# Optimization experiments

Hardware: AMD Instinct MI355X
Metric: run time of the kernel (lower is better)

## Reference

```python
import jax, jax.numpy as jnp
import numpy as np

B, T, E = 2048, 200, 128
H1, H2 = 64, 32
NEG_INF = -(2.0 ** 32) + 1.0  # matches tf source's -2**32 + 1 padding value


def setup_inputs() -> dict:
    key = jax.random.key(0)
    ks = jax.random.split(key, 8)
    queries = jax.random.normal(ks[0], (B, E), dtype=jnp.float32)
    keys = jax.random.normal(ks[1], (B, T, E), dtype=jnp.float32)
    keys_id = jax.random.randint(ks[2], (B, T), 0, 2, dtype=jnp.int32)
    # Dense params: MLP input is concat([q,k,q-k,q*k]) -> 4*E = 512
    W1 = jax.random.normal(ks[3], (4 * E, H1), dtype=jnp.float32) * (1.0 / np.sqrt(4 * E))
    b1 = jnp.zeros((H1,), dtype=jnp.float32)
    W2 = jax.random.normal(ks[4], (H1, H2), dtype=jnp.float32) * (1.0 / np.sqrt(H1))
    b2 = jnp.zeros((H2,), dtype=jnp.float32)
    W3 = jax.random.normal(ks[5], (H2, 1), dtype=jnp.float32) * (1.0 / np.sqrt(H2))
    b3 = jnp.zeros((1,), dtype=jnp.float32)
    return {"queries": queries, "keys": keys, "keys_id": keys_id,
            "W1": W1, "b1": b1, "W2": W2, "b2": b2, "W3": W3, "b3": b3}


def reference(queries, keys, keys_id, W1, b1, W2, b2, W3, b3):
    # tile query over the time axis: [B,E] -> [B,T,E]
    q = jnp.broadcast_to(queries[:, None, :], keys.shape)
    # concat features: [B,T,4E]
    feat = jnp.concatenate([q, keys, q - keys, q * keys], axis=2)
    # small MLP scorer
    h = jax.nn.relu(jnp.einsum('btf,fh->bth', feat, W1) + b1)
    h = jax.nn.relu(jnp.einsum('bth,hk->btk', h, W2) + b2)
    weight = jnp.einsum('btk,ko->bto', h, W3) + b3  # [B,T,1]
    # masked softmax over time axis (padding id == 0)
    mask = (keys_id != 0)[:, :, None]  # [B,T,1]
    weight = jnp.where(mask, weight, jnp.float32(NEG_INF))
    weight = jax.nn.softmax(weight, axis=1)
    # weighted mean pooling (original uses reduce_mean, i.e. sum/T)
    return jnp.mean(weight * keys, axis=1)  # [B,E]
```

## Files before the change

kernel.cpp:

```cpp
#include <hip/hip_runtime.h>

#define NEG_INF_F (-4294967295.0f)

typedef __attribute__((ext_vector_type(8))) short bf16x8;
typedef __attribute__((ext_vector_type(4))) float f32x4;

__device__ __forceinline__ unsigned short f2bf(float x) {
    unsigned u = __float_as_uint(x);
    unsigned r = (u + 0x7fffu + ((u >> 16) & 1u)) >> 16;
    return (unsigned short)r;
}
__device__ __forceinline__ float bf2f(unsigned short s) {
    return __uint_as_float(((unsigned)s) << 16);
}

struct __align__(16) Smem {
    unsigned short K[200 * 128];
    unsigned short h1s[4][16 * 64];
    float q[128];
    float maskf[208];
    float cpart[256];
    float s[208];
    float ppart[128];
    float red[16];
};
static_assert(sizeof(Smem) <= 64 * 1024, "LDS over 64 KiB");

__global__ __launch_bounds__(256, 2)
void attn_fused(const float* __restrict__ Q,
                const float* __restrict__ Kg,
                const int*   __restrict__ kid,
                const float* __restrict__ W1,
                const float* __restrict__ b1,
                const float* __restrict__ W2,
                const float* __restrict__ b2,
                const float* __restrict__ W3,
                const float* __restrict__ b3,
                float* __restrict__ out)
{
    __shared__ Smem sm;
    const int b    = blockIdx.x;
    const int tid  = threadIdx.x;
    const int wave = tid >> 6;
    const int lane = tid & 63;
    const int l15  = lane & 15;
    const int quad = lane >> 4;

    if (tid < 128) sm.q[tid] = Q[b * 128 + tid];
    if (tid < 200) sm.maskf[tid] = (kid[b * 200 + tid] != 0) ? 1.0f : 0.0f;
    __syncthreads();

    {
        const int n = tid & 63, kc = tid >> 6;
        float acc = (kc == 0) ? b1[n] : 0.0f;
        #pragma unroll 4
        for (int i = 0; i < 32; ++i) {
            const int k = kc * 32 + i;
            acc += sm.q[k] * (W1[k * 64 + n] + W1[(256 + k) * 64 + n]);
        }
        sm.cpart[kc * 64 + n] = acc;
    }

    {
        const float4* src = reinterpret_cast<const float4*>(Kg + (size_t)b * 200 * 128);
        #pragma unroll
        for (int r = 0; r < 25; ++r) {
            const int idx4 = tid + 256 * r;
            const float4 v = src[idx4];
            const int t = idx4 >> 5;
            const int e = (idx4 & 31) << 2;
            const int g = (e >> 3) ^ (t & 15);
            ushort4 pk;
            pk.x = f2bf(v.x); pk.y = f2bf(v.y); pk.z = f2bf(v.z); pk.w = f2bf(v.w);
            *reinterpret_cast<ushort4*>(&sm.K[t * 128 + g * 8 + (e & 7)]) = pk;
        }
    }
    __syncthreads();

    bf16x8 Mf[4][4];
    #pragma unroll
    for (int ks = 0; ks < 4; ++ks) {
        #pragma unroll
        for (int nt = 0; nt < 4; ++nt) {
            const int n = nt * 16 + l15;
            const int kb = ks * 32 + quad * 8;
            bf16x8 f;
            #pragma unroll
            for (int j = 0; j < 8; ++j) {
                const int k = kb + j;
                const float wb = W1[(128 + k) * 64 + n];
                const float wd = W1[(256 + k) * 64 + n];
                const float wp = W1[(384 + k) * 64 + n];
                f[j] = (short)f2bf((wb - wd) + sm.q[k] * wp);
            }
            Mf[ks][nt] = f;
        }
    }
    bf16x8 W2f[2][2];
    #pragma unroll
    for (int ks = 0; ks < 2; ++ks) {
        #pragma unroll
        for (int nt = 0; nt < 2; ++nt) {
            const int n = nt * 16 + l15;
            const int kb = ks * 32 + quad * 8;
            bf16x8 f;
            #pragma unroll
            for (int j = 0; j < 8; ++j) f[j] = (short)f2bf(W2[(kb + j) * 32 + n]);
            W2f[ks][nt] = f;
        }
    }
    const float w3a = W3[l15],  w3b = W3[16 + l15];
    const float b2a = b2[l15],  b2b = b2[16 + l15];
    const float b3v = b3[0];
    float cn[4];
    #pragma unroll
    for (int nt = 0; nt < 4; ++nt) {
        const int n = nt * 16 + l15;
        cn[nt] = sm.cpart[n] + sm.cpart[64 + n] + sm.cpart[128 + n] + sm.cpart[192 + n];
    }

    unsigned short* h1w = &sm.h1s[wave][0];
    const f32x4 zero4 = {0.f, 0.f, 0.f, 0.f};

    for (int tile = wave; tile < 13; tile += 4) {
        const int t0 = tile * 16;
        const int t  = t0 + l15;
        f32x4 acc[4] = {zero4, zero4, zero4, zero4};
        #pragma unroll
        for (int ks = 0; ks < 4; ++ks) {
            const int g = (ks * 4 + quad) ^ (t & 15);
            const bf16x8 A = *reinterpret_cast<const bf16x8*>(&sm.K[t * 128 + g * 8]);
            #pragma unroll
            for (int nt = 0; nt < 4; ++nt)
                acc[nt] = __builtin_amdgcn_mfma_f32_16x16x32_bf16(A, Mf[ks][nt], acc[nt], 0, 0, 0);
        }
        #pragma unroll
        for (int nt = 0; nt < 4; ++nt) {
            const int n = nt * 16 + l15;
            #pragma unroll
            for (int r = 0; r < 4; ++r) {
                const int m = quad * 4 + r;
                const float h = fmaxf(acc[nt][r] + cn[nt], 0.0f);
                const int g = (n >> 3) ^ (m & 7);
                h1w[m * 64 + g * 8 + (n & 7)] = f2bf(h);
            }
        }
        f32x4 p0 = zero4, p1 = zero4;
        #pragma unroll
        for (int ks = 0; ks < 2; ++ks) {
            const int g = (ks * 4 + quad) ^ (l15 & 7);
            const bf16x8 A2 = *reinterpret_cast<const bf16x8*>(&h1w[l15 * 64 + g * 8]);
            p0 = __builtin_amdgcn_mfma_f32_16x16x32_bf16(A2, W2f[ks][0], p0, 0, 0, 0);
            p1 = __builtin_amdgcn_mfma_f32_16x16x32_bf16(A2, W2f[ks][1], p1, 0, 0, 0);
        }
        float sv[4];
        #pragma unroll
        for (int r = 0; r < 4; ++r)
            sv[r] = fmaxf(p0[r] + b2a, 0.f) * w3a + fmaxf(p1[r] + b2b, 0.f) * w3b;
        #pragma unroll
        for (int off = 1; off < 16; off <<= 1) {
            #pragma unroll
            for (int r = 0; r < 4; ++r) sv[r] += __shfl_xor(sv[r], off);
        }
        if (l15 == 0) {
            #pragma unroll
            for (int r = 0; r < 4; ++r) {
                const int tt = t0 + quad * 4 + r;
                if (tt < 200)
                    sm.s[tt] = (sm.maskf[tt] != 0.0f) ? (sv[r] + b3v) : NEG_INF_F;
                else if (tt < 208)
                    sm.s[tt] = -__builtin_inff();
            }
        }
    }
    __syncthreads();

    {
        const float v = (tid < 208) ? sm.s[tid] : -__builtin_inff();
        float m = v;
        #pragma unroll
        for (int off = 32; off >= 1; off >>= 1) m = fmaxf(m, __shfl_xor(m, off));
        if (lane == 0) sm.red[wave] = m;
        __syncthreads();
        m = fmaxf(fmaxf(sm.red[0], sm.red[1]), fmaxf(sm.red[2], sm.red[3]));
        const float ev = (tid < 208) ? __expf(v - m) : 0.0f;
        float ssum = ev;
        #pragma unroll
        for (int off = 32; off >= 1; off >>= 1) ssum += __shfl_xor(ssum, off);
        if (lane == 0) sm.red[8 + wave] = ssum;
        __syncthreads();
        const float S = sm.red[8] + sm.red[9] + sm.red[10] + sm.red[11];
        const float inv = 1.0f / (S * 200.0f);
        if (tid < 208) sm.s[tid] = ev * inv;
    }
    __syncthreads();

    {
        const int e = tid & 127;
        const int h = tid >> 7;
        float acc2 = 0.0f;
        const int tbeg = h * 100;
        for (int tt = tbeg; tt < tbeg + 100; ++tt) {
            const float wv = sm.s[tt];
            const int g = (e >> 3) ^ (tt & 15);
            acc2 += wv * bf2f(sm.K[tt * 128 + g * 8 + (e & 7)]);
        }
        if (h == 1) sm.ppart[e] = acc2;
        __syncthreads();
        if (h == 0) out[(size_t)b * 128 + e] = acc2 + sm.ppart[e];
    }
}

extern "C" void kernel_launch(void* const* d_in, const int* in_sizes, int n_in,
                              void* d_out, int out_size, void* d_ws, size_t ws_size,
                              hipStream_t stream) {
    (void)in_sizes; (void)n_in; (void)out_size; (void)d_ws; (void)ws_size;
    attn_fused<<<dim3(2048), dim3(256), 0, stream>>>(
        (const float*)d_in[0], (const float*)d_in[1], (const int*)d_in[2],
        (const float*)d_in[3], (const float*)d_in[4], (const float*)d_in[5],
        (const float*)d_in[6], (const float*)d_in[7], (const float*)d_in[8],
        (float*)d_out);
}
```

Before: 354.0 us.

## Assign one batch row per wave and stream keys from global memory

Each 256-thread block now handles four batch rows, one per wave, and launches 512 blocks instead of 2048. Keys are no longer staged as bf16 in LDS; each wave reads its rows directly from global memory for both the MLP and the pooling pass. The q-dependent weight fold is replaced by a second MFMA per step on q*k against shared Wd/Wp fragments, so the weights are built once per block and shared by the four rows. Softmax runs entirely within a wave with no block barriers. The trade-off is twice the MFMA work, keys read twice from global memory or cache, and fewer blocks available to hide latency.

```diff
diff --git a/kernel.cpp b/kernel.cpp
--- a/kernel.cpp
+++ b/kernel.cpp
@@ -1,4 +1,5 @@
 #include <hip/hip_runtime.h>
+#include <hip/hip_bf16.h>
 
 #define NEG_INF_F (-4294967295.0f)
 
@@ -7,24 +8,22 @@
 
 __device__ __forceinline__ unsigned short f2bf(float x) {
     unsigned u = __float_as_uint(x);
-    unsigned r = (u + 0x7fffu + ((u >> 16) & 1u)) >> 16;
-    return (unsigned short)r;
-}
-__device__ __forceinline__ float bf2f(unsigned short s) {
-    return __uint_as_float(((unsigned)s) << 16);
-}
+    return (unsigned short)((u + 0x7fffu + ((u >> 16) & 1u)) >> 16);
+}
+__device__ __forceinline__ unsigned f2bf2(float a, float b) {
+    __hip_bfloat162 h2 = __float22bfloat162_rn(make_float2(a, b));
+    unsigned r; __builtin_memcpy(&r, &h2, 4); return r;
+}
+
+union FragU { unsigned u[4]; bf16x8 h; };
 
 struct __align__(16) Smem {
-    unsigned short K[200 * 128];
+    unsigned short Wt[2][64 * 128];
     unsigned short h1s[4][16 * 64];
-    float q[128];
-    float maskf[208];
-    float cpart[256];
-    float s[208];
-    float ppart[128];
-    float red[16];
+    float q[4][128];
+    float c[4][64];
+    float w[4][208];
 };
-static_assert(sizeof(Smem) <= 64 * 1024, "LDS over 64 KiB");
 
 __global__ __launch_bounds__(256, 2)
 void attn_fused(const float* __restrict__ Q,
@@ -39,61 +38,49 @@
                 float* __restrict__ out)
 {
     __shared__ Smem sm;
-    const int b    = blockIdx.x;
     const int tid  = threadIdx.x;
     const int wave = tid >> 6;
     const int lane = tid & 63;
     const int l15  = lane & 15;
     const int quad = lane >> 4;
-
-    if (tid < 128) sm.q[tid] = Q[b * 128 + tid];
-    if (tid < 200) sm.maskf[tid] = (kid[b * 200 + tid] != 0) ? 1.0f : 0.0f;
+    const int b    = blockIdx.x * 4 + wave;
+
+    {
+        const int n  = tid & 63;
+        const int ko = tid >> 6;
+        #pragma unroll 8
+        for (int i = 0; i < 32; ++i) {
+            const int k = i * 4 + ko;
+            const float a = W1[(128 + k) * 64 + n];
+            const float d = W1[(256 + k) * 64 + n];
+            const float p = W1[(384 + k) * 64 + n];
+            const int g = (k >> 3) ^ (n & 15);
+            sm.Wt[0][n * 128 + g * 8 + (k & 7)] = f2bf(a - d);
+            sm.Wt[1][n * 128 + g * 8 + (k & 7)] = f2bf(p);
+        }
+    }
+    sm.q[wave][lane]      = Q[b * 128 + lane];
+    sm.q[wave][64 + lane] = Q[b * 128 + 64 + lane];
     __syncthreads();
 
     {
-        const int n = tid & 63, kc = tid >> 6;
-        float acc = (kc == 0) ? b1[n] : 0.0f;
+        const int n = lane;
+        float acc = b1[n];
         #pragma unroll 4
-        for (int i = 0; i < 32; ++i) {
-            const int k = kc * 32 + i;
-            acc += sm.q[k] * (W1[k * 64 + n] + W1[(256 + k) * 64 + n]);
-        }
-        sm.cpart[kc * 64 + n] = acc;
-    }
-
-    {
-        const float4* src = reinterpret_cast<const float4*>(Kg + (size_t)b * 200 * 128);
-        #pragma unroll
-        for (int r = 0; r < 25; ++r) {
-            const int idx4 = tid + 256 * r;
-            const float4 v = src[idx4];
-            const int t = idx4 >> 5;
-            const int e = (idx4 & 31) << 2;
-            const int g = (e >> 3) ^ (t & 15);
-            ushort4 pk;
-            pk.x = f2bf(v.x); pk.y = f2bf(v.y); pk.z = f2bf(v.z); pk.w = f2bf(v.w);
-            *reinterpret_cast<ushort4*>(&sm.K[t * 128 + g * 8 + (e & 7)]) = pk;
-        }
-    }
-    __syncthreads();
-
-    bf16x8 Mf[4][4];
+        for (int k = 0; k < 128; ++k)
+            acc += sm.q[wave][k] * (W1[k * 64 + n] + W1[(256 + k) * 64 + n]);
+        sm.c[wave][n] = acc;
+    }
+
+    bf16x8 Wcf[4][4], Wpf[4][4];
     #pragma unroll
     for (int ks = 0; ks < 4; ++ks) {
         #pragma unroll
         for (int nt = 0; nt < 4; ++nt) {
             const int n = nt * 16 + l15;
-            const int kb = ks * 32 + quad * 8;
-            bf16x8 f;
-            #pragma unroll
-            for (int j = 0; j < 8; ++j) {
-                const int k = kb + j;
-                const float wb = W1[(128 + k) * 64 + n];
-                const float wd = W1[(256 + k) * 64 + n];
-                const float wp = W1[(384 + k) * 64 + n];
-                f[j] = (short)f2bf((wb - wd) + sm.q[k] * wp);
-            }
-            Mf[ks][nt] = f;
+            const int g = (ks * 4 + quad) ^ l15;
+            Wcf[ks][nt] = *reinterpret_cast<const bf16x8*>(&sm.Wt[0][n * 128 + g * 8]);
+            Wpf[ks][nt] = *reinterpret_cast<const bf16x8*>(&sm.Wt[1][n * 128 + g * 8]);
         }
     }
     bf16x8 W2f[2][2];
@@ -112,27 +99,42 @@
     const float w3a = W3[l15],  w3b = W3[16 + l15];
     const float b2a = b2[l15],  b2b = b2[16 + l15];
     const float b3v = b3[0];
+    float4 qa[4], qb[4];
+    #pragma unroll
+    for (int ks = 0; ks < 4; ++ks) {
+        const int e0 = ks * 32 + quad * 8;
+        qa[ks] = *reinterpret_cast<const float4*>(&sm.q[wave][e0]);
+        qb[ks] = *reinterpret_cast<const float4*>(&sm.q[wave][e0 + 4]);
+    }
     float cn[4];
     #pragma unroll
-    for (int nt = 0; nt < 4; ++nt) {
-        const int n = nt * 16 + l15;
-        cn[nt] = sm.cpart[n] + sm.cpart[64 + n] + sm.cpart[128 + n] + sm.cpart[192 + n];
-    }
+    for (int nt = 0; nt < 4; ++nt) cn[nt] = sm.c[wave][nt * 16 + l15];
 
     unsigned short* h1w = &sm.h1s[wave][0];
     const f32x4 zero4 = {0.f, 0.f, 0.f, 0.f};
-
-    for (int tile = wave; tile < 13; tile += 4) {
+    const float* kbase = Kg + (size_t)b * 25600;
+
+    for (int tile = 0; tile < 13; ++tile) {
         const int t0 = tile * 16;
-        const int t  = t0 + l15;
+        const int tr = min(t0 + l15, 199);
+        const float* kr = kbase + tr * 128;
         f32x4 acc[4] = {zero4, zero4, zero4, zero4};
         #pragma unroll
         for (int ks = 0; ks < 4; ++ks) {
-            const int g = (ks * 4 + quad) ^ (t & 15);
-            const bf16x8 A = *reinterpret_cast<const bf16x8*>(&sm.K[t * 128 + g * 8]);
-            #pragma unroll
-            for (int nt = 0; nt < 4; ++nt)
-                acc[nt] = __builtin_amdgcn_mfma_f32_16x16x32_bf16(A, Mf[ks][nt], acc[nt], 0, 0, 0);
+            const float4 k0 = *reinterpret_cast<const float4*>(kr + ks * 32 + quad * 8);
+            const float4 k1 = *reinterpret_cast<const float4*>(kr + ks * 32 + quad * 8 + 4);
+            FragU A1, A2;
+            A1.u[0] = f2bf2(k0.x, k0.y);           A1.u[1] = f2bf2(k0.z, k0.w);
+            A1.u[2] = f2bf2(k1.x, k1.y);           A1.u[3] = f2bf2(k1.z, k1.w);
+            A2.u[0] = f2bf2(k0.x * qa[ks].x, k0.y * qa[ks].y);
+            A2.u[1] = f2bf2(k0.z * qa[ks].z, k0.w * qa[ks].w);
+            A2.u[2] = f2bf2(k1.x * qb[ks].x, k1.y * qb[ks].y);
+            A2.u[3] = f2bf2(k1.z * qb[ks].z, k1.w * qb[ks].w);
+            #pragma unroll
+            for (int nt = 0; nt < 4; ++nt) {
+                acc[nt] = __builtin_amdgcn_mfma_f32_16x16x32_bf16(A1.h, Wcf[ks][nt], acc[nt], 0, 0, 0);
+                acc[nt] = __builtin_amdgcn_mfma_f32_16x16x32_bf16(A2.h, Wpf[ks][nt], acc[nt], 0, 0, 0);
+            }
         }
         #pragma unroll
         for (int nt = 0; nt < 4; ++nt) {
@@ -149,9 +151,9 @@
         #pragma unroll
         for (int ks = 0; ks < 2; ++ks) {
             const int g = (ks * 4 + quad) ^ (l15 & 7);
-            const bf16x8 A2 = *reinterpret_cast<const bf16x8*>(&h1w[l15 * 64 + g * 8]);
-            p0 = __builtin_amdgcn_mfma_f32_16x16x32_bf16(A2, W2f[ks][0], p0, 0, 0, 0);
-            p1 = __builtin_amdgcn_mfma_f32_16x16x32_bf16(A2, W2f[ks][1], p1, 0, 0, 0);
+            const bf16x8 A2l = *reinterpret_cast<const bf16x8*>(&h1w[l15 * 64 + g * 8]);
+            p0 = __builtin_amdgcn_mfma_f32_16x16x32_bf16(A2l, W2f[ks][0], p0, 0, 0, 0);
+            p1 = __builtin_amdgcn_mfma_f32_16x16x32_bf16(A2l, W2f[ks][1], p1, 0, 0, 0);
         }
         float sv[4];
         #pragma unroll
@@ -164,50 +166,60 @@
         }
         if (l15 == 0) {
             #pragma unroll
-            for (int r = 0; r < 4; ++r) {
-                const int tt = t0 + quad * 4 + r;
-                if (tt < 200)
-                    sm.s[tt] = (sm.maskf[tt] != 0.0f) ? (sv[r] + b3v) : NEG_INF_F;
-                else if (tt < 208)
-                    sm.s[tt] = -__builtin_inff();
+            for (int r = 0; r < 4; ++r) sm.w[wave][t0 + quad * 4 + r] = sv[r];
+        }
+    }
+
+    {
+        const float NINF = -__builtin_inff();
+        float v[4];
+        #pragma unroll
+        for (int i = 0; i < 4; ++i) {
+            const int t = lane + i * 64;
+            float x = NINF;
+            if (t < 200) {
+                const float raw = sm.w[wave][t];
+                x = (kid[b * 200 + t] != 0) ? (raw + b3v) : NEG_INF_F;
             }
-        }
-    }
-    __syncthreads();
-
-    {
-        const float v = (tid < 208) ? sm.s[tid] : -__builtin_inff();
-        float m = v;
-        #pragma unroll
-        for (int off = 32; off >= 1; off >>= 1) m = fmaxf(m, __shfl_xor(m, off));
-        if (lane == 0) sm.red[wave] = m;
-        __syncthreads();
-        m = fmaxf(fmaxf(sm.red[0], sm.red[1]), fmaxf(sm.red[2], sm.red[3]));
-        const float ev = (tid < 208) ? __expf(v - m) : 0.0f;
-        float ssum = ev;
-        #pragma unroll
-        for (int off = 32; off >= 1; off >>= 1) ssum += __shfl_xor(ssum, off);
-        if (lane == 0) sm.red[8 + wave] = ssum;
-        __syncthreads();
-        const float S = sm.red[8] + sm.red[9] + sm.red[10] + sm.red[11];
+            v[i] = x;
+        }
+        float m = fmaxf(fmaxf(v[0], v[1]), fmaxf(v[2], v[3]));
+        #pragma unroll
+        for (int off = 1; off < 64; off <<= 1) m = fmaxf(m, __shfl_xor(m, off));
+        float e[4], S = 0.f;
+        #pragma unroll
+        for (int i = 0; i < 4; ++i) { e[i] = __expf(v[i] - m); S += e[i]; }
+        #pragma unroll
+        for (int off = 1; off < 64; off <<= 1) S += __shfl_xor(S, off);
         const float inv = 1.0f / (S * 200.0f);
-        if (tid < 208) sm.s[tid] = ev * inv;
-    }
-    __syncthreads();
-
-    {
-        const int e = tid & 127;
-        const int h = tid >> 7;
-        float acc2 = 0.0f;
-        const int tbeg = h * 100;
-        for (int tt = tbeg; tt < tbeg + 100; ++tt) {
-            const float wv = sm.s[tt];
-            const int g = (e >> 3) ^ (tt & 15);
-            acc2 += wv * bf2f(sm.K[tt * 128 + g * 8 + (e & 7)]);
-        }
-        if (h == 1) sm.ppart[e] = acc2;
-        __syncthreads();
-        if (h == 0) out[(size_t)b * 128 + e] = acc2 + sm.ppart[e];
+        #pragma unroll
+        for (int i = 0; i < 4; ++i) {
+            const int t = lane + i * 64;
+            if (t < 208) sm.w[wave][t] = e[i] * inv;
+        }
+    }
+
+    {
+        const int e2 = lane * 2;
+        const float* kp = kbase + e2;
+        float ax0 = 0.f, ay0 = 0.f, ax1 = 0.f, ay1 = 0.f;
+        float ax2 = 0.f, ay2 = 0.f, ax3 = 0.f, ay3 = 0.f;
+        #pragma unroll 5
+        for (int t = 0; t < 200; t += 4) {
+            const float4 wv = *reinterpret_cast<const float4*>(&sm.w[wave][t]);
+            const float2 x0 = *reinterpret_cast<const float2*>(kp + (t + 0) * 128);
+            const float2 x1 = *reinterpret_cast<const float2*>(kp + (t + 1) * 128);
+            const float2 x2 = *reinterpret_cast<const float2*>(kp + (t + 2) * 128);
+            const float2 x3 = *reinterpret_cast<const float2*>(kp + (t + 3) * 128);
+            ax0 += wv.x * x0.x; ay0 += wv.x * x0.y;
+            ax1 += wv.y * x1.x; ay1 += wv.y * x1.y;
+            ax2 += wv.z * x2.x; ay2 += wv.z * x2.y;
+            ax3 += wv.w * x3.x; ay3 += wv.w * x3.y;
+        }
+        float2 o;
+        o.x = (ax0 + ax1) + (ax2 + ax3);
+        o.y = (ay0 + ay1) + (ay2 + ay3);
+        *reinterpret_cast<float2*>(&out[(size_t)b * 128 + e2]) = o;
     }
 }
 
@@ -215,7 +227,7 @@
                               void* d_out, int out_size, void* d_ws, size_t ws_size,
                               hipStream_t stream) {
     (void)in_sizes; (void)n_in; (void)out_size; (void)d_ws; (void)ws_size;
-    attn_fused<<<dim3(2048), dim3(256), 0, stream>>>(
+    attn_fused<<<dim3(512), dim3(256), 0, stream>>>(
         (const float*)d_in[0], (const float*)d_in[1], (const int*)d_in[2],
         (const float*)d_in[3], (const float*)d_in[4], (const float*)d_in[5],
         (const float*)d_in[6], (const float*)d_in[7], (const float*)d_in[8],
```

Result: faster. 346.8 us (-2.0%).
